# Optimization experiments

Hardware: AMD Instinct MI355X
Metric: run time of the kernel (lower is better)

## Reference

```python
import jax, jax.numpy as jnp
import numpy as np
import math

D_MODEL = 1024
NUM_HEADS = 16
HEAD_DIM = D_MODEL // NUM_HEADS
ROPE_THETA = 10000.0
MAX_SEQ_LEN = 4096


def setup_inputs() -> dict:
    key = jax.random.key(0)
    ks = jax.random.split(key, 6)
    sigma = math.sqrt(2.0 / (D_MODEL + D_MODEL))
    def w(k):
        # trunc_normal within [-3sigma, 3sigma] ~ approximate with clipped normal
        return jnp.clip(sigma * jax.random.normal(k, (D_MODEL, D_MODEL), dtype=jnp.float32), -3 * sigma, 3 * sigma)
    x = jax.random.normal(ks[0], (2, 2048, D_MODEL), dtype=jnp.float32)
    token_positions = jnp.arange(2048, dtype=jnp.int64 if jax.config.jax_enable_x64 else jnp.int32)
    return {
        "x": x,
        "wq": w(ks[1]),
        "wk": w(ks[2]),
        "wv": w(ks[3]),
        "wo": w(ks[4]),
        "token_positions": token_positions,
    }


def _rope(t, positions):
    # t: (B, H, S, head_dim); positions: (S,)
    half = HEAD_DIM // 2
    inv_freq = 1.0 / (ROPE_THETA ** (jnp.arange(0, HEAD_DIM, 2, dtype=jnp.float32) / HEAD_DIM))  # (half,)
    freqs = positions.astype(jnp.float32)[:, None] * inv_freq[None, :]  # (S, half)
    cos = jnp.cos(freqs)
    sin = jnp.sin(freqs)
    t_even = t[..., ::2]   # (B,H,S,half)
    t_odd = t[..., 1::2]
    rot_even = t_even * cos - t_odd * sin
    rot_odd = t_even * sin + t_odd * cos
    return jnp.stack([rot_even, rot_odd], axis=-1).reshape(t.shape)


def reference(x, wq, wk, wv, wo, token_positions):
    B, S, _ = x.shape
    def split_heads(t):
        return t.reshape(B, S, NUM_HEADS, HEAD_DIM).transpose(0, 2, 1, 3)  # (B,H,S,Dh)
    q = split_heads(jnp.einsum('bsd,ed->bse', x, wq))
    k = split_heads(jnp.einsum('bsd,ed->bse', x, wk))
    v = split_heads(jnp.einsum('bsd,ed->bse', x, wv))
    q = _rope(q, token_positions)
    k = _rope(k, token_positions)
    scores = jnp.einsum('bhqd,bhkd->bhqk', q, k) / math.sqrt(HEAD_DIM)
    causal = jnp.tril(jnp.ones((S, S), dtype=bool))
    scores = jnp.where(causal, scores, -jnp.inf)
    probs = jax.nn.softmax(scores, axis=-1)
    out = jnp.einsum('bhqk,bhkd->bhqd', probs, v)  # (B,H,S,Dh)
    out = out.transpose(0, 2, 1, 3).reshape(B, S, D_MODEL)
    return jnp.einsum('bsd,ed->bse', out, wo)
```

## Files before the change

### kernel.cpp

```cpp
#include <hip/hip_runtime.h>
#include <hip/hip_bf16.h>


#define D_MODEL 1024
#define NHEADS  16
#define HDIM    64
#define SEQ     2048
#define BATCH   2

typedef unsigned short u16;
typedef __bf16 bf16x8_t __attribute__((ext_vector_type(8)));
typedef float  f32x4_t  __attribute__((ext_vector_type(4)));

__device__ __forceinline__ u16 f2bf(float f) {
    union { __hip_bfloat16 h; u16 u; } cv;
    cv.h = __float2bfloat16(f);
    return cv.u;
}

__device__ __forceinline__ unsigned pk2(float x, float y) {
    union { __hip_bfloat162 h; unsigned u; } cv;
    cv.h = __float22bfloat162_rn(make_float2(x, y));
    return cv.u;
}

__device__ __forceinline__ uint4 pack8(float4 a, float4 b) {
    uint4 u;
    u.x = pk2(a.x, a.y);
    u.y = pk2(a.z, a.w);
    u.z = pk2(b.x, b.y);
    u.w = pk2(b.z, b.w);
    return u;
}

__device__ __forceinline__ bf16x8_t frag_ld(const u16* p) {
    union { uint4 u; bf16x8_t v; } t;
    t.u = *(const uint4*)p;
    return t.v;
}

__device__ __forceinline__ void acc8(uint4 u, float* a) {
    a[0] += __uint_as_float(u.x << 16); a[1] += __uint_as_float(u.x & 0xffff0000u);
    a[2] += __uint_as_float(u.y << 16); a[3] += __uint_as_float(u.y & 0xffff0000u);
    a[4] += __uint_as_float(u.z << 16); a[5] += __uint_as_float(u.z & 0xffff0000u);
    a[6] += __uint_as_float(u.w << 16); a[7] += __uint_as_float(u.w & 0xffff0000u);
}

__device__ __forceinline__ void dma16(const u16* g, u16* l) {
    __builtin_amdgcn_global_load_lds(
        (const __attribute__((address_space(1))) void*)g,
        (__attribute__((address_space(3))) void*)l, 16, 0, 0);
}

__global__ __launch_bounds__(256) void conv_bf16_kernel(
    const float* __restrict__ X, const float* __restrict__ Wq,
    const float* __restrict__ Wk, const float* __restrict__ Wv,
    const float* __restrict__ Wo, u16* __restrict__ Xbf, u16* __restrict__ Wbf)
{
    const size_t gid = (size_t)blockIdx.x * 256 + threadIdx.x;
    const float* src;
    u16* dst;
    size_t off;
    if (gid < (1u << 19)) {
        src = X; dst = Xbf; off = gid;
    } else {
        size_t g = gid - (1u << 19);
        const int wsel = (int)(g >> 17);
        g &= (1u << 17) - 1;
        src = (wsel == 0) ? Wq : (wsel == 1) ? Wk : (wsel == 2) ? Wv : Wo;
        dst = Wbf + ((size_t)wsel << 20);
        off = g;
    }
    const float4 a = *(const float4*)(src + off * 8);
    const float4 b = *(const float4*)(src + off * 8 + 4);
    *(uint4*)(dst + off * 8) = pack8(a, b);
}

__global__ __launch_bounds__(256) void qkv_rope_kernel(
    const u16* __restrict__ Xbf, const u16* __restrict__ Wbf,
    const int* __restrict__ pos,
    u16* __restrict__ Qo, u16* __restrict__ Ko, u16* __restrict__ Vt)
{
    __shared__ __align__(16) u16 smem[32768];
    const int tid = threadIdx.x;
    const int m0 = blockIdx.y * 128;
    const int nv = blockIdx.x * 128;
    const int which = nv >> 10;
    const int nbase = nv & 1023;
    const u16* __restrict__ Wsrc = Wbf + ((size_t)which << 20);

    const int w = tid >> 6, L = tid & 63, quad = L >> 4, colL = L & 15;
    const int mw = (w & 1) * 64, nw = (w >> 1) * 64;

    const int lrow = L >> 3;
    const int lchk = (L & 7) ^ lrow;
    const u16* ag = Xbf + (size_t)(m0 + 32 * w + lrow) * D_MODEL + lchk * 8;
    const u16* bg = Wsrc + (size_t)(nbase + 32 * w + lrow) * D_MODEL + lchk * 8;

    f32x4_t acc[4][4];
    #pragma unroll
    for (int i = 0; i < 4; ++i)
        #pragma unroll
        for (int j = 0; j < 4; ++j) acc[i][j] = (f32x4_t){0.f, 0.f, 0.f, 0.f};

    #define QKV_STAGE(boff, k0)                                                 \
        {                                                                       \
            u16* al = smem + (boff) + (32 * w) * 64;                            \
            u16* bl = smem + 16384 + (boff) + (32 * w) * 64;                    \
            _Pragma("unroll")                                                   \
            for (int j = 0; j < 4; ++j) {                                       \
                dma16(ag + (size_t)j * 8 * D_MODEL + (k0), al + j * 512);       \
                dma16(bg + (size_t)j * 8 * D_MODEL + (k0), bl + j * 512);       \
            }                                                                   \
        }

    QKV_STAGE(0, 0)
    for (int it = 0; it < 16; ++it) {
        const int boff = (it & 1) << 13;
        if (it < 15) {
            QKV_STAGE(boff ^ 8192, (it + 1) * 64)
            asm volatile("s_waitcnt vmcnt(8)" ::: "memory");
        } else {
            asm volatile("s_waitcnt vmcnt(0)" ::: "memory");
        }
        __builtin_amdgcn_sched_barrier(0);
        __builtin_amdgcn_s_barrier();
        __builtin_amdgcn_sched_barrier(0);

        const u16* a_s = smem + boff;
        const u16* b_s = smem + 16384 + boff;
        #pragma unroll
        for (int kb = 0; kb < 2; ++kb) {
            const int ch = ((kb * 4 + quad) ^ (colL & 7)) * 8;
            bf16x8_t af[4], bf[4];
            #pragma unroll
            for (int t = 0; t < 4; ++t) {
                af[t] = frag_ld(a_s + (mw + t * 16 + colL) * 64 + ch);
                bf[t] = frag_ld(b_s + (nw + t * 16 + colL) * 64 + ch);
            }
            #pragma unroll
            for (int mt = 0; mt < 4; ++mt)
                #pragma unroll
                for (int nt = 0; nt < 4; ++nt)
                    acc[mt][nt] = __builtin_amdgcn_mfma_f32_16x16x32_bf16(
                        af[mt], bf[nt], acc[mt][nt], 0, 0, 0);
        }
        __builtin_amdgcn_s_barrier();
    }

    __syncthreads();
    u16 (*Ts)[132] = (u16(*)[132])smem;

    const float C0 = 0.14391156831212787f;
    if (which < 2) {
        const float oscale = (which == 0) ? 0.18033688011112042f : 1.0f;
        float invf[4], sgn[4];
        #pragma unroll
        for (int nt = 0; nt < 4; ++nt) {
            const int n = nbase + nw + nt * 16 + colL;
            const int dd = n & 63;
            invf[nt] = __expf(-(float)(dd & 62) * C0);
            sgn[nt] = (dd & 1) ? 1.0f : -1.0f;
        }
        #pragma unroll
        for (int mt = 0; mt < 4; ++mt) {
            #pragma unroll
            for (int r = 0; r < 4; ++r) {
                const int ml = mw + mt * 16 + quad * 4 + r;
                const int ss = (m0 + ml) & 2047;
                const float p = (float)pos[ss];
                #pragma unroll
                for (int nt = 0; nt < 4; ++nt) {
                    const float v = acc[mt][nt][r];
                    const float partner = __shfl_xor(v, 1);
                    float sn, cs;
                    __sincosf(p * invf[nt], &sn, &cs);
                    Ts[ml][nw + nt * 16 + colL] =
                        f2bf((v * cs + sgn[nt] * sn * partner) * oscale);
                }
            }
        }
    } else {
        #pragma unroll
        for (int mt = 0; mt < 4; ++mt)
            #pragma unroll
            for (int nt = 0; nt < 4; ++nt)
                #pragma unroll
                for (int r = 0; r < 4; ++r)
                    Ts[nw + nt * 16 + colL][mw + mt * 16 + quad * 4 + r] = f2bf(acc[mt][nt][r]);
    }
    __syncthreads();

    const int rr0 = tid >> 4;
    const int cc8 = (tid & 15) * 8;
    if (which < 2) {
        u16* __restrict__ dst = (which == 0) ? Qo : Ko;
        #pragma unroll
        for (int it = 0; it < 8; ++it) {
            const int ml = rr0 + it * 16;
            const int m = m0 + ml, bb = m >> 11, ss = m & 2047;
            const int n = nbase + cc8, h = n >> 6, d = n & 63;
            *(uint4*)&dst[((size_t)(bb * NHEADS + h) * SEQ + ss) * HDIM + d] =
                *(const uint4*)&Ts[ml][cc8];
        }
    } else {
        const int bb = m0 >> 11, ss0 = (m0 & 2047) + cc8;
        #pragma unroll
        for (int it = 0; it < 8; ++it) {
            const int nl = rr0 + it * 16;
            const int n = nbase + nl, h = n >> 6, d = n & 63;
            *(uint4*)&Vt[((size_t)(bb * NHEADS + h) * HDIM + d) * SEQ + ss0] =
                *(const uint4*)&Ts[nl][cc8];
        }
    }
}

__global__ __launch_bounds__(256) void attn_kernel(
    const u16* __restrict__ Q, const u16* __restrict__ K,
    const u16* __restrict__ Vt, u16* __restrict__ Opart, float* __restrict__ Lpart)
{
    __shared__ __align__(16) u16 Ks[64][64];
    __shared__ __align__(16) u16 Vs[64][64];
    __shared__ __align__(16) u16 Ps[4][16][64];

    const int tid = threadIdx.x;
    const int slot = 79 - (int)blockIdx.x;
    const int g = (slot >= 48) ? 3 : (slot >= 24) ? 2 : (slot >= 8) ? 1 : 0;
    const int t0 = slot - 4 * g * (g + 1);
    const int rr = t0 / (g + 1);
    const int s  = t0 - rr * (g + 1);
    const int qt = 8 * g + rr;

    const int hh = blockIdx.y, bb = blockIdx.z;
    const size_t bh = ((size_t)bb * NHEADS + hh) * (SEQ * HDIM);
    const int q0 = qt * 64;
    const int kt0 = s * 8;
    const int ktend = min(kt0 + 8, qt + 1);
    const size_t gslot = ((size_t)(bb * NHEADS + hh) * 80 + slot);

    const int w = tid >> 6, L = tid & 63, quad = L >> 4, colL = L & 15;
    const int srow = tid >> 2, sc = (tid & 3) * 16;
    const int c7 = colL & 7;
    const int sch0 = (((tid & 3) * 2) ^ (srow & 7)) * 8;
    const int sch1 = (((tid & 3) * 2 + 1) ^ (srow & 7)) * 8;

    const u16* qp = Q + bh + (size_t)(q0 + w * 16 + colL) * HDIM + quad * 8;
    const bf16x8_t aq0 = frag_ld(qp);
    const bf16x8_t aq1 = frag_ld(qp + 32);

    float lsum = 0.f;
    f32x4_t O[4];
    #pragma unroll
    for (int dt = 0; dt < 4; ++dt) O[dt] = (f32x4_t){0.f, 0.f, 0.f, 0.f};

    const u16* kp = K + bh + (size_t)(kt0 * 64 + srow) * HDIM + sc;
    const u16* vp = Vt + bh + (size_t)srow * SEQ + kt0 * 64 + sc;
    uint4 kv0 = *(const uint4*)kp;
    uint4 kv1 = *(const uint4*)(kp + 8);
    uint4 vv0 = *(const uint4*)vp;
    uint4 vv1 = *(const uint4*)(vp + 8);

    for (int kt = kt0; kt < ktend; ++kt) {
        __builtin_amdgcn_s_barrier();
        asm volatile("s_waitcnt vmcnt(0)" ::: "memory");
        __builtin_amdgcn_sched_barrier(0);
        *(uint4*)&Ks[srow][sch0] = kv0;
        *(uint4*)&Ks[srow][sch1] = kv1;
        *(uint4*)&Vs[srow][sch0] = vv0;
        *(uint4*)&Vs[srow][sch1] = vv1;
        if (kt + 1 < ktend) {
            const int k1 = (kt + 1) * 64;
            const u16* kpn = K + bh + (size_t)(k1 + srow) * HDIM + sc;
            kv0 = *(const uint4*)kpn;
            kv1 = *(const uint4*)(kpn + 8);
            const u16* vpn = Vt + bh + (size_t)srow * SEQ + k1 + sc;
            vv0 = *(const uint4*)vpn;
            vv1 = *(const uint4*)(vpn + 8);
        }
        asm volatile("s_waitcnt lgkmcnt(0)" ::: "memory");
        __builtin_amdgcn_sched_barrier(0);
        __builtin_amdgcn_s_barrier();

        const bool diag = (kt == qt);
        const int ntmax = diag ? w : 3;
        const int kbmax = diag ? (w >> 1) : 1;

        f32x4_t S[4];
        #pragma unroll
        for (int nt = 0; nt < 4; ++nt) S[nt] = (f32x4_t){0.f, 0.f, 0.f, 0.f};
        #pragma unroll
        for (int nt = 0; nt < 4; ++nt) {
            if (nt <= ntmax) {
                S[nt] = __builtin_amdgcn_mfma_f32_16x16x32_bf16(
                    frag_ld(&Ks[nt * 16 + colL][(quad ^ c7) * 8]), aq0, S[nt], 0, 0, 0);
                S[nt] = __builtin_amdgcn_mfma_f32_16x16x32_bf16(
                    frag_ld(&Ks[nt * 16 + colL][((quad ^ 4) ^ c7) * 8]), aq1, S[nt], 0, 0, 0);
            }
        }

        if (!diag) {
            #pragma unroll
            for (int nt = 0; nt < 4; ++nt) {
                const float p0 = __builtin_amdgcn_exp2f(S[nt][0]);
                const float p1 = __builtin_amdgcn_exp2f(S[nt][1]);
                const float p2 = __builtin_amdgcn_exp2f(S[nt][2]);
                const float p3 = __builtin_amdgcn_exp2f(S[nt][3]);
                lsum += (p0 + p1) + (p2 + p3);
                uint2 pw;
                pw.x = pk2(p0, p1);
                pw.y = pk2(p2, p3);
                *(uint2*)&Ps[w][colL][((2 * nt + (quad >> 1)) ^ c7) * 8 + (quad & 1) * 4] = pw;
            }
        } else {
            const int qrel = w * 16 + colL;
            #pragma unroll
            for (int nt = 0; nt < 4; ++nt) {
                float p0 = 0.f, p1 = 0.f, p2 = 0.f, p3 = 0.f;
                if (nt <= ntmax) {
                    const int krel = nt * 16 + quad * 4;
                    p0 = (krel + 0 <= qrel) ? __builtin_amdgcn_exp2f(S[nt][0]) : 0.f;
                    p1 = (krel + 1 <= qrel) ? __builtin_amdgcn_exp2f(S[nt][1]) : 0.f;
                    p2 = (krel + 2 <= qrel) ? __builtin_amdgcn_exp2f(S[nt][2]) : 0.f;
                    p3 = (krel + 3 <= qrel) ? __builtin_amdgcn_exp2f(S[nt][3]) : 0.f;
                }
                lsum += (p0 + p1) + (p2 + p3);
                uint2 pw;
                pw.x = pk2(p0, p1);
                pw.y = pk2(p2, p3);
                *(uint2*)&Ps[w][colL][((2 * nt + (quad >> 1)) ^ c7) * 8 + (quad & 1) * 4] = pw;
            }
        }

        asm volatile("s_waitcnt lgkmcnt(0)" ::: "memory");
        __builtin_amdgcn_sched_barrier(0);

        #pragma unroll
        for (int kb = 0; kb < 2; ++kb) {
            if (kb <= kbmax) {
                const int ch = ((kb * 4 + quad) ^ c7) * 8;
                const bf16x8_t ap = frag_ld(&Ps[w][colL][ch]);
                #pragma unroll
                for (int dt = 0; dt < 4; ++dt) {
                    const bf16x8_t bv = frag_ld(&Vs[dt * 16 + colL][ch]);
                    O[dt] = __builtin_amdgcn_mfma_f32_16x16x32_bf16(ap, bv, O[dt], 0, 0, 0);
                }
            }
        }
    }

    {
        float sm = lsum;
        sm += __shfl_xor(sm, 16);
        sm += __shfl_xor(sm, 32);
        if (quad == 0)
            Lpart[gslot * 64 + 16 * w + colL] = sm;
    }

    #pragma unroll
    for (int dt = 0; dt < 4; ++dt)
        #pragma unroll
        for (int r = 0; r < 4; ++r) {
            const int row = quad * 4 + r;
            const int ch = ((2 * dt + (colL >> 3)) ^ (row & 7)) * 8 + (colL & 7);
            Ps[w][row][ch] = f2bf(O[dt][r]);
        }
    asm volatile("s_waitcnt lgkmcnt(0)" ::: "memory");
    __builtin_amdgcn_sched_barrier(0);
    #pragma unroll
    for (int p = 0; p < 2; ++p) {
        const int rowl = (L >> 3) + 8 * p;
        const int ch = ((L & 7) ^ (rowl & 7)) * 8;
        *(uint4*)&Opart[gslot * 4096 + (size_t)(16 * w + rowl) * 64 + (L & 7) * 8] =
            *(const uint4*)&Ps[w][rowl][ch];
    }
}

__global__ __launch_bounds__(256) void combine_kernel(
    const u16* __restrict__ Opart, const float* __restrict__ Lpart,
    u16* __restrict__ AO)
{
    const int qt = blockIdx.x, hh = blockIdx.y, bb = blockIdx.z;
    const int g = qt >> 3;
    const int nsplit = g + 1;
    const int base = 4 * g * (g + 1) + (qt & 7) * (g + 1);
    const int t = threadIdx.x;
    const int q = t >> 2, dg = (t & 3) * 16;
    const size_t slot0 = (size_t)(bb * NHEADS + hh) * 80 + base;

    float acc[16];
    #pragma unroll
    for (int i = 0; i < 16; ++i) acc[i] = 0.f;
    float l = 0.f;
    for (int s = 0; s < nsplit; ++s) {
        const size_t gs = slot0 + s;
        l += Lpart[gs * 64 + q];
        const u16* op = Opart + gs * 4096 + (size_t)q * 64 + dg;
        acc8(*(const uint4*)op, acc);
        acc8(*(const uint4*)(op + 8), acc + 8);
    }
    const float inv = 1.0f / l;
    uint4 o0, o1;
    o0.x = pk2(acc[0] * inv, acc[1] * inv);  o0.y = pk2(acc[2] * inv, acc[3] * inv);
    o0.z = pk2(acc[4] * inv, acc[5] * inv);  o0.w = pk2(acc[6] * inv, acc[7] * inv);
    o1.x = pk2(acc[8] * inv, acc[9] * inv);  o1.y = pk2(acc[10] * inv, acc[11] * inv);
    o1.z = pk2(acc[12] * inv, acc[13] * inv); o1.w = pk2(acc[14] * inv, acc[15] * inv);
    u16* dst = AO + ((size_t)bb * SEQ + qt * 64 + q) * D_MODEL + hh * HDIM + dg;
    *(uint4*)dst = o0;
    *(uint4*)(dst + 8) = o1;
}

__global__ __launch_bounds__(256) void out_proj_kernel(
    const u16* __restrict__ A, const u16* __restrict__ Wob, float* __restrict__ Out)
{
    __shared__ __align__(16) u16 smem[24576];

    const int tid = threadIdx.x;
    const int m0 = blockIdx.y * 64;
    const int n0 = blockIdx.x * 128;

    const int w = tid >> 6, L = tid & 63, quad = L >> 4, colL = L & 15;
    const int mw = (w & 1) * 32, nw = (w >> 1) * 64;

    const int lrow = L >> 3;
    const int lchk = (L & 7) ^ lrow;

    f32x4_t acc[2][4];
    #pragma unroll
    for (int i = 0; i < 2; ++i)
        #pragma unroll
        for (int j = 0; j < 4; ++j) acc[i][j] = (f32x4_t){0.f, 0.f, 0.f, 0.f};

    #define OP_STAGE(boff, k0)                                                  \
        {                                                                       \
            _Pragma("unroll")                                                   \
            for (int j = 0; j < 6; ++j) {                                       \
                const int R0 = 48 * w + 8 * j;                                  \
                const u16* src = (R0 < 64)                                      \
                    ? A + (size_t)(m0 + R0 + lrow) * D_MODEL + lchk * 8         \
                    : Wob + (size_t)(n0 + R0 - 64 + lrow) * D_MODEL + lchk * 8; \
                dma16(src + (k0), smem + (boff) + R0 * 64);                     \
            }                                                                   \
        }

    OP_STAGE(0, 0)
    for (int it = 0; it < 16; ++it) {
        const int boff = (it & 1) * 12288;
        if (it < 15) {
            OP_STAGE(boff ^ 12288, (it + 1) * 64)
            asm volatile("s_waitcnt vmcnt(6)" ::: "memory");
        } else {
            asm volatile("s_waitcnt vmcnt(0)" ::: "memory");
        }
        __builtin_amdgcn_sched_barrier(0);
        __builtin_amdgcn_s_barrier();
        __builtin_amdgcn_sched_barrier(0);

        const u16* a_s = smem + boff;
        const u16* b_s = smem + boff + 4096;
        #pragma unroll
        for (int kb = 0; kb < 2; ++kb) {
            const int ch = ((kb * 4 + quad) ^ (colL & 7)) * 8;
            bf16x8_t af[2], bf[4];
            #pragma unroll
            for (int t = 0; t < 2; ++t)
                af[t] = frag_ld(a_s + (mw + t * 16 + colL) * 64 + ch);
            #pragma unroll
            for (int t = 0; t < 4; ++t)
                bf[t] = frag_ld(b_s + (nw + t * 16 + colL) * 64 + ch);
            #pragma unroll
            for (int mt = 0; mt < 2; ++mt)
                #pragma unroll
                for (int nt = 0; nt < 4; ++nt)
                    acc[mt][nt] = __builtin_amdgcn_mfma_f32_16x16x32_bf16(
                        af[mt], bf[nt], acc[mt][nt], 0, 0, 0);
        }
        __builtin_amdgcn_s_barrier();
    }

    #pragma unroll
    for (int mt = 0; mt < 2; ++mt)
        #pragma unroll
        for (int nt = 0; nt < 4; ++nt)
            #pragma unroll
            for (int r = 0; r < 4; ++r) {
                const int m = m0 + mw + mt * 16 + quad * 4 + r;
                const int n = n0 + nw + nt * 16 + colL;
                Out[(size_t)m * D_MODEL + n] = acc[mt][nt][r];
            }
}

extern "C" void kernel_launch(void* const* d_in, const int* in_sizes, int n_in,
                              void* d_out, int out_size, void* d_ws, size_t ws_size,
                              hipStream_t stream) {
    const float* x  = (const float*)d_in[0];
    const float* wq = (const float*)d_in[1];
    const float* wk = (const float*)d_in[2];
    const float* wv = (const float*)d_in[3];
    const float* wo = (const float*)d_in[4];
    const int* pos  = (const int*)d_in[5];
    float* out = (float*)d_out;

    const size_t NELEM = (size_t)BATCH * NHEADS * SEQ * HDIM;
    u16* Qw  = (u16*)d_ws;
    u16* Kw  = Qw + NELEM;
    u16* Vtw = Kw + NELEM;
    u16* AOw = Vtw + NELEM;
    u16* Xbf = AOw;
    u16* Wbf = AOw + NELEM;
    u16* Opart = Wbf + NELEM;
    float* Lpart = (float*)(Opart + (size_t)2560 * 4096);

    conv_bf16_kernel<<<4096, 256, 0, stream>>>(x, wq, wk, wv, wo, Xbf, Wbf);
    qkv_rope_kernel<<<dim3(24, 32), 256, 0, stream>>>(Xbf, Wbf, pos, Qw, Kw, Vtw);
    attn_kernel<<<dim3(80, NHEADS, BATCH), 256, 0, stream>>>(Qw, Kw, Vtw, Opart, Lpart);
    combine_kernel<<<dim3(32, NHEADS, BATCH), 256, 0, stream>>>(Opart, Lpart, AOw);
    out_proj_kernel<<<dim3(8, 64), 256, 0, stream>>>(AOw, Wbf + 3 * (1u << 20), out);
}
```

Baseline: 185.0 us.

## Fuse split-KV combine into output projection A-tile staging

Removes the separate combine kernel. The output projection now reads the partial attention outputs and row sums directly, reduces them in registers, normalises them and writes the bf16 A tile into shared memory for each K step (one head per 64-wide K chunk). This saves a launch and the write and re-read of the AO buffer. In exchange, each of the 8 N-column blocks repeats the combine work for its rows, and the pipeline now waits on vmcnt(0) at every iteration, which may weaken the overlap between loads and compute.

Result: slower. 192.0 us (+3.8%).

```diff
diff --git a/kernel.cpp b/kernel.cpp
--- a/kernel.cpp
+++ b/kernel.cpp
@@ -375,42 +375,9 @@
     }
 }
 
-__global__ __launch_bounds__(256) void combine_kernel(
+__global__ __launch_bounds__(256) void out_proj_kernel(
     const u16* __restrict__ Opart, const float* __restrict__ Lpart,
-    u16* __restrict__ AO)
-{
-    const int qt = blockIdx.x, hh = blockIdx.y, bb = blockIdx.z;
-    const int g = qt >> 3;
-    const int nsplit = g + 1;
-    const int base = 4 * g * (g + 1) + (qt & 7) * (g + 1);
-    const int t = threadIdx.x;
-    const int q = t >> 2, dg = (t & 3) * 16;
-    const size_t slot0 = (size_t)(bb * NHEADS + hh) * 80 + base;
-
-    float acc[16];
-    #pragma unroll
-    for (int i = 0; i < 16; ++i) acc[i] = 0.f;
-    float l = 0.f;
-    for (int s = 0; s < nsplit; ++s) {
-        const size_t gs = slot0 + s;
-        l += Lpart[gs * 64 + q];
-        const u16* op = Opart + gs * 4096 + (size_t)q * 64 + dg;
-        acc8(*(const uint4*)op, acc);
-        acc8(*(const uint4*)(op + 8), acc + 8);
-    }
-    const float inv = 1.0f / l;
-    uint4 o0, o1;
-    o0.x = pk2(acc[0] * inv, acc[1] * inv);  o0.y = pk2(acc[2] * inv, acc[3] * inv);
-    o0.z = pk2(acc[4] * inv, acc[5] * inv);  o0.w = pk2(acc[6] * inv, acc[7] * inv);
-    o1.x = pk2(acc[8] * inv, acc[9] * inv);  o1.y = pk2(acc[10] * inv, acc[11] * inv);
-    o1.z = pk2(acc[12] * inv, acc[13] * inv); o1.w = pk2(acc[14] * inv, acc[15] * inv);
-    u16* dst = AO + ((size_t)bb * SEQ + qt * 64 + q) * D_MODEL + hh * HDIM + dg;
-    *(uint4*)dst = o0;
-    *(uint4*)(dst + 8) = o1;
-}
-
-__global__ __launch_bounds__(256) void out_proj_kernel(
-    const u16* __restrict__ A, const u16* __restrict__ Wob, float* __restrict__ Out)
+    const u16* __restrict__ Wob, float* __restrict__ Out)
 {
     __shared__ __align__(16) u16 smem[24576];
 
@@ -424,33 +391,86 @@
     const int lrow = L >> 3;
     const int lchk = (L & 7) ^ lrow;
 
+    const int bb = m0 >> 11;
+    const int qt = (m0 & 2047) >> 6;
+    const int cg_ = qt >> 3;
+    const int nsplit = cg_ + 1;
+    const int base = 4 * cg_ * (cg_ + 1) + (qt & 7) * (cg_ + 1);
+    const int bb16 = bb * NHEADS;
+
+    const u16* bg = Wob + (size_t)(n0 + 32 * w + lrow) * D_MODEL + lchk * 8;
+
     f32x4_t acc[2][4];
     #pragma unroll
     for (int i = 0; i < 2; ++i)
         #pragma unroll
         for (int j = 0; j < 4; ++j) acc[i][j] = (f32x4_t){0.f, 0.f, 0.f, 0.f};
 
-    #define OP_STAGE(boff, k0)                                                  \
+    uint4 ldo[2][4];
+    float ldl[2][4];
+
+    #define A_ISSUE(hs)                                                         \
+        {                                                                       \
+            const size_t slot0 = ((size_t)(bb16 + (hs))) * 80 + base;           \
+            _Pragma("unroll")                                                   \
+            for (int c = 0; c < 2; ++c) {                                       \
+                const int slot = tid + 256 * c;                                 \
+                const int q = slot >> 3, cg = slot & 7;                         \
+                _Pragma("unroll")                                               \
+                for (int s = 0; s < 4; ++s) {                                   \
+                    if (s < nsplit) {                                           \
+                        const size_t gs = slot0 + s;                            \
+                        ldo[c][s] = *(const uint4*)(Opart + gs * 4096 +         \
+                                                    (size_t)q * 64 + cg * 8);   \
+                        ldl[c][s] = Lpart[gs * 64 + q];                         \
+                    }                                                           \
+                }                                                               \
+            }                                                                   \
+        }
+
+    #define A_WRITE(boff)                                                       \
         {                                                                       \
             _Pragma("unroll")                                                   \
-            for (int j = 0; j < 6; ++j) {                                       \
-                const int R0 = 48 * w + 8 * j;                                  \
-                const u16* src = (R0 < 64)                                      \
-                    ? A + (size_t)(m0 + R0 + lrow) * D_MODEL + lchk * 8         \
-                    : Wob + (size_t)(n0 + R0 - 64 + lrow) * D_MODEL + lchk * 8; \
-                dma16(src + (k0), smem + (boff) + R0 * 64);                     \
+            for (int c = 0; c < 2; ++c) {                                       \
+                const int slot = tid + 256 * c;                                 \
+                const int q = slot >> 3, cg = slot & 7;                         \
+                float o[8];                                                     \
+                _Pragma("unroll")                                               \
+                for (int i = 0; i < 8; ++i) o[i] = 0.f;                         \
+                float l = 0.f;                                                  \
+                _Pragma("unroll")                                               \
+                for (int s = 0; s < 4; ++s)                                     \
+                    if (s < nsplit) { acc8(ldo[c][s], o); l += ldl[c][s]; }     \
+                const float inv = 1.0f / l;                                     \
+                uint4 pw;                                                       \
+                pw.x = pk2(o[0] * inv, o[1] * inv);                             \
+                pw.y = pk2(o[2] * inv, o[3] * inv);                             \
+                pw.z = pk2(o[4] * inv, o[5] * inv);                             \
+                pw.w = pk2(o[6] * inv, o[7] * inv);                             \
+                *(uint4*)&smem[(boff) + q * 64 + ((cg ^ (q & 7)) * 8)] = pw;    \
             }                                                                   \
         }
 
-    OP_STAGE(0, 0)
+    #define B_ISSUE(boff, k0)                                                   \
+        {                                                                       \
+            u16* bl = smem + (boff) + 4096 + (32 * w) * 64;                     \
+            _Pragma("unroll")                                                   \
+            for (int j = 0; j < 4; ++j)                                         \
+                dma16(bg + (size_t)j * 8 * D_MODEL + (k0), bl + j * 512);       \
+        }
+
+    A_ISSUE(0)
+    B_ISSUE(0, 0)
     for (int it = 0; it < 16; ++it) {
         const int boff = (it & 1) * 12288;
+        asm volatile("s_waitcnt vmcnt(0)" ::: "memory");
+        __builtin_amdgcn_sched_barrier(0);
+        A_WRITE(boff)
         if (it < 15) {
-            OP_STAGE(boff ^ 12288, (it + 1) * 64)
-            asm volatile("s_waitcnt vmcnt(6)" ::: "memory");
-        } else {
-            asm volatile("s_waitcnt vmcnt(0)" ::: "memory");
-        }
+            A_ISSUE(it + 1)
+            B_ISSUE(boff ^ 12288, (it + 1) * 64)
+        }
+        asm volatile("s_waitcnt lgkmcnt(0)" ::: "memory");
         __builtin_amdgcn_sched_barrier(0);
         __builtin_amdgcn_s_barrier();
         __builtin_amdgcn_sched_barrier(0);
@@ -513,6 +533,5 @@
     conv_bf16_kernel<<<4096, 256, 0, stream>>>(x, wq, wk, wv, wo, Xbf, Wbf);
     qkv_rope_kernel<<<dim3(24, 32), 256, 0, stream>>>(Xbf, Wbf, pos, Qw, Kw, Vtw);
     attn_kernel<<<dim3(80, NHEADS, BATCH), 256, 0, stream>>>(Qw, Kw, Vtw, Opart, Lpart);
-    combine_kernel<<<dim3(32, NHEADS, BATCH), 256, 0, stream>>>(Opart, Lpart, AOw);
-    out_proj_kernel<<<dim3(8, 64), 256, 0, stream>>>(AOw, Wbf + 3 * (1u << 20), out);
-}
+    out_proj_kernel<<<dim3(8, 64), 256, 0, stream>>>(Opart, Lpart, Wbf + 3 * (1u << 20), out);
+}
```
